# Performance work log

Measured on AMD Instinct MI355X. Metric: run time of the kernel, lower is better.

The kernel has to match this reference:

```python
import jax, jax.numpy as jnp
import numpy as np

N_WIN = 8  # matches init kwarg n_win

def setup_inputs() -> dict:
    key = jax.random.key(0)
    k1, k2, k3 = jax.random.split(key, 3)
    c = 64
    x = jax.random.normal(k1, (1, c, 256, 256), dtype=jnp.float32)
    W = jax.random.normal(k2, (3 * c, c), dtype=jnp.float32) * 0.05
    bias = jax.random.normal(k3, (3 * c,), dtype=jnp.float32) * 0.05
    return {"x": x, "W": W, "bias": bias}

def reference(x, W, bias):
    b, c, h, w = x.shape
    n_h = n_w = N_WIN
    hs, ws = h // n_h, w // n_w
    nw = n_h * n_w
    # unfold into non-overlapping windows: [1, nw, hs*ws, c]
    xw = x.reshape(b, c, n_h, hs, n_w, ws)
    xw = xw.transpose(0, 2, 4, 3, 5, 1).reshape(1, nw, hs * ws, c)
    # shared QKV linear
    qkv = xw @ W.T + bias
    q, k, v = qkv[..., :c], qkv[..., c:2 * c], qkv[..., 2 * c:3 * c]
    # region-level routing via mean-pooled tokens
    q_r = q.mean(axis=2)  # [1, nw, c]
    k_r = k.mean(axis=2)
    a_r = jax.nn.relu(jnp.einsum('bic,bjc->bij', q_r, k_r))  # [1, nw, nw]
    # mix windows: a_r @ flattened(k/q) == window-mixing einsum
    k_m = jnp.einsum('bij,bjtc->bitc', a_r, k)
    q_m = jnp.einsum('bij,bjtc->bitc', a_r, q)
    # relu-gated windowed attention
    attn = jax.nn.relu(jnp.einsum('bitc,bisc->bits', q_m, k_m))  # [1, nw, T, T]
    o = jnp.einsum('bits,bisc->bitc', attn, v)  # [1, nw, T, c]
    # fold back to image
    o = o.reshape(b, n_h, n_w, hs, ws, c).transpose(0, 5, 1, 3, 2, 4).reshape(b, c, h, w)
    return o
```

## Files before the change

kernel.cpp:

```cpp
#include <hip/hip_runtime.h>

typedef _Float16 half_t;
typedef __attribute__((ext_vector_type(8))) _Float16 half8;
typedef __attribute__((ext_vector_type(4))) _Float16 half4;
typedef __attribute__((ext_vector_type(4))) float floatx4;
typedef __attribute__((ext_vector_type(16))) float floatx16;

#define MFMA16(A, B, C) __builtin_amdgcn_mfma_f32_16x16x32_f16((A), (B), (C), 0, 0, 0)
#define MFMA32(A, B, C) __builtin_amdgcn_mfma_f32_32x32x16_f16((A), (B), (C), 0, 0, 0)

__global__ __launch_bounds__(256) void k_qkv(
    const float* __restrict__ x, const float* __restrict__ W,
    const float* __restrict__ bias, half_t* __restrict__ q,
    half_t* __restrict__ k, half_t* __restrict__ vT,
    float* __restrict__ qsum, float* __restrict__ ksum) {
  __shared__ __align__(16) char smem[52736];
  half_t(*Xs)[72] = (half_t(*)[72])smem;
  half_t(*Ws)[72] = (half_t(*)[72])(smem + 18432);
  half_t(*S1)[136] = (half_t(*)[136])smem;
  half_t(*S2)[136] = (half_t(*)[136])(smem + 34816);
  float* qs_l = (float*)(smem + 52224);
  float* ks_l = qs_l + 64;
  const int w = blockIdx.y;
  const int tx = blockIdx.x;
  const int t0 = tx * 128;
  const int ih = w >> 3, iw = w & 7;
  const int xbase = ih * 8192 + iw * 32 + tx * 1024;
  const int tid = threadIdx.x;

  for (int i = tid; i < 2048; i += 256) {
    const int c = i >> 5, g = i & 31;
    const int tt = (g >> 3) * 32 + (g & 7) * 4;
    const floatx4 v =
        *(const floatx4*)&x[c * 65536 + xbase + (g >> 3) * 256 + (g & 7) * 4];
    #pragma unroll
    for (int p = 0; p < 4; p++) Xs[tt + p][c] = (half_t)v[p];
  }
  for (int i = tid; i < 3072; i += 256) {
    const int o = i >> 4, c4 = (i & 15) * 4;
    const floatx4 v = *(const floatx4*)&W[o * 64 + c4];
    half4 hv;
    #pragma unroll
    for (int p = 0; p < 4; p++) hv[p] = (half_t)v[p];
    *(half4*)&Ws[o][c4] = hv;
  }
  if (tid < 64) { qs_l[tid] = 0.f; ks_l[tid] = 0.f; }
  __syncthreads();

  const int wave = tid >> 6, lane = tid & 63;
  const int lrow = lane & 15, lq = lane >> 4;
  const int rbase = (wave >> 1) * 64;
  const int cbase = (wave & 1) * 96;

  floatx4 acc[4][6];
  const floatx4 z = {0.f, 0.f, 0.f, 0.f};
  #pragma unroll
  for (int mt = 0; mt < 4; mt++)
    #pragma unroll
    for (int nt = 0; nt < 6; nt++) acc[mt][nt] = z;

  #pragma unroll
  for (int kf = 0; kf < 2; kf++) {
    const int koff = kf * 32 + lq * 8;
    half8 a[4], b[6];
    #pragma unroll
    for (int mt = 0; mt < 4; mt++)
      a[mt] = *(const half8*)&Xs[rbase + mt * 16 + lrow][koff];
    #pragma unroll
    for (int nt = 0; nt < 6; nt++)
      b[nt] = *(const half8*)&Ws[cbase + nt * 16 + lrow][koff];
    #pragma unroll
    for (int mt = 0; mt < 4; mt++)
      #pragma unroll
      for (int nt = 0; nt < 6; nt++)
        acc[mt][nt] = MFMA16(a[mt], b[nt], acc[mt][nt]);
  }
  __syncthreads();

  #pragma unroll
  for (int nt = 0; nt < 6; nt++) {
    const int o = cbase + nt * 16 + lrow;
    const float bs = bias[o];
    if (o < 128) {
      float s = 0.f;
      #pragma unroll
      for (int mt = 0; mt < 4; mt++) {
        const int tr = rbase + mt * 16 + lq * 4;
        #pragma unroll
        for (int r = 0; r < 4; r++) {
          const float v = acc[mt][nt][r] + bs;
          S1[tr + r][o] = (half_t)v;
          s += v;
        }
      }
      if (o < 64) atomicAdd(&qs_l[o], s);
      else atomicAdd(&ks_l[o - 64], s);
    } else {
      const int oc = o - 128;
      #pragma unroll
      for (int mt = 0; mt < 4; mt++) {
        const int tr = rbase + mt * 16 + lq * 4;
        half4 pk;
        #pragma unroll
        for (int r = 0; r < 4; r++) pk[r] = (half_t)(acc[mt][nt][r] + bs);
        *(half4*)&S2[oc][tr] = pk;
      }
    }
  }
  __syncthreads();

  for (int idx = tid; idx < 3072; idx += 256) {
    if (idx < 2048) {
      const int t = idx >> 4, seg = idx & 15;
      const half8 v = *(const half8*)&S1[t][seg * 8];
      if (seg < 8)
        *(half8*)&q[w * 65536 + (t0 + t) * 64 + seg * 8] = v;
      else
        *(half8*)&k[w * 65536 + (t0 + t) * 64 + (seg - 8) * 8] = v;
    } else {
      const int i2 = idx - 2048;
      const int oc = i2 >> 4, seg = i2 & 15;
      *(half8*)&vT[w * 65536 + oc * 1024 + t0 + seg * 8] =
          *(const half8*)&S2[oc][seg * 8];
    }
  }
  if (tid < 64) {
    atomicAdd(&qsum[w * 64 + tid], qs_l[tid]);
    atomicAdd(&ksum[w * 64 + tid], ks_l[tid]);
  }
}

__global__ __launch_bounds__(256) void k_mix(const half_t* __restrict__ q,
                                             const half_t* __restrict__ k,
                                             const float* __restrict__ qsum,
                                             const float* __restrict__ ksum,
                                             half_t* __restrict__ qm,
                                             half_t* __restrict__ km) {
  __shared__ __align__(16) half_t qh[64][72];
  __shared__ __align__(16) half_t kh[64][72];
  __shared__ __align__(16) half_t arL[64][72];
  const half_t* __restrict__ src = blockIdx.y ? k : q;
  half_t* __restrict__ dst = blockIdx.y ? km : qm;
  const int tid = threadIdx.x;
  const int wave = tid >> 6, lane = tid & 63;
  const int ln31 = lane & 31;
  const int hk8 = (lane >> 5) * 8;
  const int lrow = lane & 15, lq = lane >> 4;

  const int pos0 = blockIdx.x * 256 + wave * 64 + ln31;
  half8 bB[2][4];
  #pragma unroll
  for (int t32 = 0; t32 < 2; t32++)
    #pragma unroll
    for (int kk = 0; kk < 4; kk++)
      #pragma unroll
      for (int jj = 0; jj < 8; jj++)
        bB[t32][kk][jj] =
            src[(kk * 16 + hk8 + jj) * 65536 + pos0 + t32 * 32];

  for (int e = tid; e < 1024; e += 256) {
    const int i = e >> 4, c4 = (e & 15) * 4;
    const floatx4 sq = *(const floatx4*)&qsum[i * 64 + c4];
    const floatx4 sk = *(const floatx4*)&ksum[i * 64 + c4];
    #pragma unroll
    for (int p = 0; p < 4; p++) {
      qh[i][c4 + p] = (half_t)sq[p];
      kh[i][c4 + p] = (half_t)sk[p];
    }
  }
  __syncthreads();

  {
    floatx4 ac[4];
    const floatx4 z = {0.f, 0.f, 0.f, 0.f};
    #pragma unroll
    for (int nt = 0; nt < 4; nt++) ac[nt] = z;
    #pragma unroll
    for (int kf = 0; kf < 2; kf++) {
      const int koff = kf * 32 + lq * 8;
      const half8 aF = *(const half8*)&qh[wave * 16 + lrow][koff];
      #pragma unroll
      for (int nt = 0; nt < 4; nt++) {
        const half8 bF = *(const half8*)&kh[nt * 16 + lrow][koff];
        ac[nt] = MFMA16(aF, bF, ac[nt]);
      }
    }
    const float scale = 1.f / (1024.f * 1024.f);
    #pragma unroll
    for (int nt = 0; nt < 4; nt++)
      #pragma unroll
      for (int r = 0; r < 4; r++) {
        const float v = ac[nt][r] * scale;
        arL[wave * 16 + lq * 4 + r][nt * 16 + lrow] =
            (half_t)(v > 0.f ? v : 0.f);
      }
  }
  __syncthreads();

  half8 aA[2][4];
  #pragma unroll
  for (int mt = 0; mt < 2; mt++)
    #pragma unroll
    for (int kk = 0; kk < 4; kk++)
      aA[mt][kk] = *(const half8*)&arL[mt * 32 + ln31][kk * 16 + hk8];

  #pragma unroll
  for (int t32 = 0; t32 < 2; t32++) {
    const int pos = pos0 + t32 * 32;
    floatx16 c0, c1;
    #pragma unroll
    for (int r = 0; r < 16; r++) { c0[r] = 0.f; c1[r] = 0.f; }
    #pragma unroll
    for (int kk = 0; kk < 4; kk++) {
      c0 = MFMA32(aA[0][kk], bB[t32][kk], c0);
      c1 = MFMA32(aA[1][kk], bB[t32][kk], c1);
    }
    const int h4 = (lane >> 5) * 4;
    #pragma unroll
    for (int r = 0; r < 16; r++) {
      const int row = (r & 3) + h4 + 8 * (r >> 2);
      dst[row * 65536 + pos] = (half_t)c0[r];
      dst[(32 + row) * 65536 + pos] = (half_t)c1[r];
    }
  }
}

__global__ __launch_bounds__(256, 3) void k_attn(const half_t* __restrict__ qm,
                                                 const half_t* __restrict__ km,
                                                 const half_t* __restrict__ vT,
                                                 float* __restrict__ out) {
  __shared__ __align__(16) char smem[34816];
  char* const VsB = smem;
  char* const StB = smem + 17408;
  const int w = blockIdx.x;
  const int t0 = blockIdx.y * 64;
  const int tid = threadIdx.x;
  const int wave = tid >> 6, lane = tid & 63;
  const int ln31 = lane & 31;
  const int hk8 = (lane >> 5) * 8, hk4 = (lane >> 5) * 4;
  const int w32 = wave * 32;
  const int wc = (wave & 1) * 32;
  const int wt = (wave >> 1) * 32;
  const int wbase = w * 65536;

  auto vs_ptr = [&](int c, int sbyte) -> char* {
    return VsB + c * 272 + (sbyte ^ ((c & 15) << 4));
  };
  auto st_ptr = [&](int t, int sbyte) -> char* {
    return StB + t * 272 + (sbyte ^ ((t & 15) << 4));
  };

  half8 bQ[2][4];
  #pragma unroll
  for (int tt = 0; tt < 2; tt++)
    #pragma unroll
    for (int kk = 0; kk < 4; kk++)
      bQ[tt][kk] = *(const half8*)&qm[wbase + (t0 + tt * 32 + ln31) * 64 +
                                      kk * 16 + hk8];

  floatx16 oacc;
  #pragma unroll
  for (int r = 0; r < 16; r++) oacc[r] = 0.f;

  half8 vpre[4], aK[4];
  #pragma unroll
  for (int j = 0; j < 4; j++) {
    const int idx = j * 256 + tid;
    const int c = idx >> 4, so = (idx & 15) * 8;
    vpre[j] = *(const half8*)&vT[wbase + c * 1024 + so];
  }
  #pragma unroll
  for (int kk = 0; kk < 4; kk++)
    aK[kk] = *(const half8*)&km[wbase + (w32 + ln31) * 64 + kk * 16 + hk8];

  for (int sc = 0; sc < 8; sc++) {
    floatx16 sacc[2];
    #pragma unroll
    for (int tt = 0; tt < 2; tt++)
      #pragma unroll
      for (int r = 0; r < 16; r++) sacc[tt][r] = 0.f;
    __builtin_amdgcn_s_setprio(1);
    #pragma unroll
    for (int kk = 0; kk < 4; kk++)
      #pragma unroll
      for (int tt = 0; tt < 2; tt++)
        sacc[tt] = MFMA32(aK[kk], bQ[tt][kk], sacc[tt]);
    __builtin_amdgcn_s_setprio(0);

    __syncthreads();

    #pragma unroll
    for (int j = 0; j < 4; j++) {
      const int idx = j * 256 + tid;
      const int c = idx >> 4;
      *(half8*)vs_ptr(c, (idx & 15) * 16) = vpre[j];
    }
    #pragma unroll
    for (int tt = 0; tt < 2; tt++) {
      const int t = tt * 32 + ln31;
      #pragma unroll
      for (int g = 0; g < 4; g++) {
        const int s = w32 + g * 8 + hk4;
        half4 pk;
        #pragma unroll
        for (int p = 0; p < 4; p++) {
          const float v = sacc[tt][g * 4 + p];
          pk[p] = (half_t)(v > 0.f ? v : 0.f);
        }
        *(half4*)st_ptr(t, s * 2) = pk;
      }
    }
    half8 aKn[4];
    if (sc < 7) {
      const int s0n = (sc + 1) * 128;
      #pragma unroll
      for (int j = 0; j < 4; j++) {
        const int idx = j * 256 + tid;
        const int c = idx >> 4, so = (idx & 15) * 8;
        vpre[j] = *(const half8*)&vT[wbase + c * 1024 + s0n + so];
      }
      #pragma unroll
      for (int kk = 0; kk < 4; kk++)
        aKn[kk] = *(const half8*)&km[wbase + (s0n + w32 + ln31) * 64 +
                                     kk * 16 + hk8];
    }
    __syncthreads();

    __builtin_amdgcn_s_setprio(1);
    #pragma unroll
    for (int kk = 0; kk < 8; kk++) {
      const half8 bS = *(const half8*)st_ptr(wt + ln31, (kk * 16 + hk8) * 2);
      const half8 aV = *(const half8*)vs_ptr(wc + ln31, (kk * 16 + hk8) * 2);
      oacc = MFMA32(aV, bS, oacc);
    }
    __builtin_amdgcn_s_setprio(0);
    if (sc < 7) {
      #pragma unroll
      for (int kk = 0; kk < 4; kk++) aK[kk] = aKn[kk];
    }
  }

  const int ih = w >> 3, iw = w & 7;
  const int obase = ih * 8192 + iw * 32;
  const int tb = ((t0 + wt) >> 5) * 256 + ln31;
  const int h4 = (lane >> 5) * 4;
  #pragma unroll
  for (int r = 0; r < 16; r++) {
    const int c = wc + (r & 3) + h4 + 8 * (r >> 2);
    out[c * 65536 + obase + tb] = oacc[r];
  }
}

extern "C" void kernel_launch(void* const* d_in, const int* in_sizes, int n_in,
                              void* d_out, int out_size, void* d_ws, size_t ws_size,
                              hipStream_t stream) {
  const float* x = (const float*)d_in[0];
  const float* W = (const float*)d_in[1];
  const float* bias = (const float*)d_in[2];
  float* out = (float*)d_out;

  half_t* q = (half_t*)d_ws;
  half_t* k = q + 4194304;
  half_t* vT = k + 4194304;
  half_t* qm = vT + 4194304;
  half_t* km = qm + 4194304;
  float* qsum = (float*)(km + 4194304);
  float* ksum = qsum + 4096;

  hipMemsetAsync(qsum, 0, 2 * 4096 * sizeof(float), stream);
  k_qkv<<<dim3(8, 64), 256, 0, stream>>>(x, W, bias, q, k, vT, qsum, ksum);
  k_mix<<<dim3(256, 2), 256, 0, stream>>>(q, k, qsum, ksum, qm, km);
  k_attn<<<dim3(64, 16), 256, 0, stream>>>(qm, km, vT, out);
}
```

Measured before the change: 142.4 us.

## Merge q/k mixing per block, relax attention barriers, widen LDS row stride

k_mix now handles both q and k for one 128-position slice in each block, instead of splitting q and k across grid.y. The routing matrix is computed once per block and reused for both MFMA sets. In k_attn, __syncthreads is replaced with a custom barrier that waits only on LDS counters (lgkmcnt), so outstanding global prefetches of V and K no longer block at the barrier. The LDS row pitch also changes from 272 to 288 bytes, which alters bank mapping at the cost of slightly more shared memory.

```diff
diff --git a/kernel.cpp b/kernel.cpp
--- a/kernel.cpp
+++ b/kernel.cpp
@@ -8,6 +8,12 @@
 
 #define MFMA16(A, B, C) __builtin_amdgcn_mfma_f32_16x16x32_f16((A), (B), (C), 0, 0, 0)
 #define MFMA32(A, B, C) __builtin_amdgcn_mfma_f32_32x32x16_f16((A), (B), (C), 0, 0, 0)
+
+__device__ __forceinline__ void lds_barrier() {
+  __builtin_amdgcn_sched_barrier(0);
+  asm volatile("s_waitcnt lgkmcnt(0)\n\ts_barrier" ::: "memory");
+  __builtin_amdgcn_sched_barrier(0);
+}
 
 __global__ __launch_bounds__(256) void k_qkv(
     const float* __restrict__ x, const float* __restrict__ W,
@@ -139,24 +145,22 @@
   __shared__ __align__(16) half_t qh[64][72];
   __shared__ __align__(16) half_t kh[64][72];
   __shared__ __align__(16) half_t arL[64][72];
-  const half_t* __restrict__ src = blockIdx.y ? k : q;
-  half_t* __restrict__ dst = blockIdx.y ? km : qm;
   const int tid = threadIdx.x;
   const int wave = tid >> 6, lane = tid & 63;
   const int ln31 = lane & 31;
   const int hk8 = (lane >> 5) * 8;
   const int lrow = lane & 15, lq = lane >> 4;
 
-  const int pos0 = blockIdx.x * 256 + wave * 64 + ln31;
-  half8 bB[2][4];
-  #pragma unroll
-  for (int t32 = 0; t32 < 2; t32++)
-    #pragma unroll
-    for (int kk = 0; kk < 4; kk++)
-      #pragma unroll
-      for (int jj = 0; jj < 8; jj++)
-        bB[t32][kk][jj] =
-            src[(kk * 16 + hk8 + jj) * 65536 + pos0 + t32 * 32];
+  const int pos = blockIdx.x * 128 + wave * 32 + ln31;
+  half8 bBq[4], bBk[4];
+  #pragma unroll
+  for (int kk = 0; kk < 4; kk++)
+    #pragma unroll
+    for (int jj = 0; jj < 8; jj++) {
+      const int off = (kk * 16 + hk8 + jj) * 65536 + pos;
+      bBq[kk][jj] = q[off];
+      bBk[kk][jj] = k[off];
+    }
 
   for (int e = tid; e < 1024; e += 256) {
     const int i = e >> 4, c4 = (e & 15) * 4;
@@ -204,24 +208,24 @@
     for (int kk = 0; kk < 4; kk++)
       aA[mt][kk] = *(const half8*)&arL[mt * 32 + ln31][kk * 16 + hk8];
 
-  #pragma unroll
-  for (int t32 = 0; t32 < 2; t32++) {
-    const int pos = pos0 + t32 * 32;
-    floatx16 c0, c1;
-    #pragma unroll
-    for (int r = 0; r < 16; r++) { c0[r] = 0.f; c1[r] = 0.f; }
-    #pragma unroll
-    for (int kk = 0; kk < 4; kk++) {
-      c0 = MFMA32(aA[0][kk], bB[t32][kk], c0);
-      c1 = MFMA32(aA[1][kk], bB[t32][kk], c1);
-    }
-    const int h4 = (lane >> 5) * 4;
-    #pragma unroll
-    for (int r = 0; r < 16; r++) {
-      const int row = (r & 3) + h4 + 8 * (r >> 2);
-      dst[row * 65536 + pos] = (half_t)c0[r];
-      dst[(32 + row) * 65536 + pos] = (half_t)c1[r];
-    }
+  floatx16 c0, c1, d0, d1;
+  #pragma unroll
+  for (int r = 0; r < 16; r++) { c0[r] = 0.f; c1[r] = 0.f; d0[r] = 0.f; d1[r] = 0.f; }
+  #pragma unroll
+  for (int kk = 0; kk < 4; kk++) {
+    c0 = MFMA32(aA[0][kk], bBq[kk], c0);
+    c1 = MFMA32(aA[1][kk], bBq[kk], c1);
+    d0 = MFMA32(aA[0][kk], bBk[kk], d0);
+    d1 = MFMA32(aA[1][kk], bBk[kk], d1);
+  }
+  const int h4 = (lane >> 5) * 4;
+  #pragma unroll
+  for (int r = 0; r < 16; r++) {
+    const int row = (r & 3) + h4 + 8 * (r >> 2);
+    qm[row * 65536 + pos] = (half_t)c0[r];
+    qm[(32 + row) * 65536 + pos] = (half_t)c1[r];
+    km[row * 65536 + pos] = (half_t)d0[r];
+    km[(32 + row) * 65536 + pos] = (half_t)d1[r];
   }
 }
 
@@ -229,9 +233,9 @@
                                                  const half_t* __restrict__ km,
                                                  const half_t* __restrict__ vT,
                                                  float* __restrict__ out) {
-  __shared__ __align__(16) char smem[34816];
+  __shared__ __align__(16) char smem[36864];
   char* const VsB = smem;
-  char* const StB = smem + 17408;
+  char* const StB = smem + 18432;
   const int w = blockIdx.x;
   const int t0 = blockIdx.y * 64;
   const int tid = threadIdx.x;
@@ -244,10 +248,10 @@
   const int wbase = w * 65536;
 
   auto vs_ptr = [&](int c, int sbyte) -> char* {
-    return VsB + c * 272 + (sbyte ^ ((c & 15) << 4));
+    return VsB + c * 288 + (sbyte ^ ((c & 15) << 4));
   };
   auto st_ptr = [&](int t, int sbyte) -> char* {
-    return StB + t * 272 + (sbyte ^ ((t & 15) << 4));
+    return StB + t * 288 + (sbyte ^ ((t & 15) << 4));
   };
 
   half8 bQ[2][4];
@@ -287,7 +291,7 @@
         sacc[tt] = MFMA32(aK[kk], bQ[tt][kk], sacc[tt]);
     __builtin_amdgcn_s_setprio(0);
 
-    __syncthreads();
+    lds_barrier();
 
     #pragma unroll
     for (int j = 0; j < 4; j++) {
@@ -324,7 +328,7 @@
         aKn[kk] = *(const half8*)&km[wbase + (s0n + w32 + ln31) * 64 +
                                      kk * 16 + hk8];
     }
-    __syncthreads();
+    lds_barrier();
 
     __builtin_amdgcn_s_setprio(1);
     #pragma unroll
@@ -369,6 +373,6 @@
 
   hipMemsetAsync(qsum, 0, 2 * 4096 * sizeof(float), stream);
   k_qkv<<<dim3(8, 64), 256, 0, stream>>>(x, W, bias, q, k, vT, qsum, ksum);
-  k_mix<<<dim3(256, 2), 256, 0, stream>>>(q, k, qsum, ksum, qm, km);
+  k_mix<<<512, 256, 0, stream>>>(q, k, qsum, ksum, qm, km);
   k_attn<<<dim3(64, 16), 256, 0, stream>>>(qm, km, vT, out);
 }
```

New measurement: 123.9 us. 1.15x faster.
